# Optimization experiments

Measured on AMD Instinct MI355X. Metric: run time of the kernel, lower is better.

The kernel has to match this reference:

```python
import math
import jax, jax.numpy as jnp
import numpy as np

B, N, D, H = 16, 256, 1024, 16
DK = D // H
LAM_ATT, LAM_DIST = 0.33, 0.33
LAM_ADJ = 1.0 - LAM_ATT - LAM_DIST
EPS, NEG_INF = 1e-6, 1e12


def setup_inputs() -> dict:
    key = jax.random.key(0)
    ks = jax.random.split(key, 16)
    inp = {
        'query': jax.random.normal(ks[0], (B, N, D), jnp.float32),
        'key': jax.random.normal(ks[1], (B, N, D), jnp.float32),
        'value': jax.random.normal(ks[2], (B, N, D), jnp.float32),
        'adj_matrix': jax.random.uniform(ks[3], (B, N, N), jnp.float32),
        'distance_matrix': jax.random.uniform(ks[4], (B, N, N), jnp.float32),
        'edges_att': jnp.zeros((1,), jnp.float32),  # unused by forward
    }
    mask = jax.random.randint(ks[5], (B, N), 0, 2, jnp.int32)
    inp['mask'] = mask.at[:, 0].set(1)  # guarantee >=1 valid atom per graph
    scale = 0.02
    inp['Wq'] = jax.random.normal(ks[6], (D, D), jnp.float32) * scale
    inp['bq'] = jnp.zeros((D,), jnp.float32)
    inp['Wk'] = jax.random.normal(ks[7], (D, D), jnp.float32) * scale
    inp['bk'] = jnp.zeros((D,), jnp.float32)
    inp['Wv'] = jax.random.normal(ks[8], (D, D), jnp.float32) * scale
    inp['bv'] = jnp.zeros((D,), jnp.float32)
    inp['Wo'] = jax.random.normal(ks[9], (D, D), jnp.float32) * scale
    inp['bo'] = jnp.zeros((D,), jnp.float32)
    return inp


def reference(query, key, value, adj_matrix, distance_matrix, edges_att, mask,
              Wq, bq, Wk, bk, Wv, bv, Wo, bo):
    b, n, d = query.shape
    proj = lambda x, W, bias: (x @ W + bias).reshape(b, n, H, DK).transpose(0, 2, 1, 3)
    q = proj(query, Wq, bq)   # [B,H,N,DK]
    k = proj(key, Wk, bk)
    v = proj(value, Wv, bv)

    scores = jnp.einsum('bhqd,bhkd->bhqk', q, k) / math.sqrt(DK)
    key_invalid = (mask == 0)[:, None, None, :]          # [B,1,1,N]
    scores = jnp.where(key_invalid, -NEG_INF, scores)
    p_attn = jax.nn.softmax(scores, axis=-1)             # [B,H,N,N]

    # row-normalized adjacency (broadcast over heads instead of repeat)
    p_adj = adj_matrix / (adj_matrix.sum(axis=-1, keepdims=True) + EPS)  # [B,N,N]

    # distance kernel: softmax(-dist) with masked columns sent to +inf
    dist = jnp.where((mask == 0)[:, None, :], jnp.inf, distance_matrix)  # [B,N,N]
    p_dist = jax.nn.softmax(-dist, axis=-1)

    p_weighted = (LAM_ATT * p_attn
                  + LAM_DIST * p_dist[:, None]
                  + LAM_ADJ * p_adj[:, None])            # [B,H,N,N]
    # dropout p=0.0 -> identity

    x = jnp.einsum('bhqk,bhkd->bhqd', p_weighted, v)     # [B,H,N,DK]
    x = x.transpose(0, 2, 1, 3).reshape(b, n, d)
    return x @ Wo + bo
```

## Files before the change

### kernel.cpp

```cpp
#include <hip/hip_runtime.h>
#include <hip/hip_bf16.h>

typedef short short8 __attribute__((ext_vector_type(8)));
typedef short short4v __attribute__((ext_vector_type(4)));
typedef float floatx4 __attribute__((ext_vector_type(4)));

constexpr int BB  = 16;
constexpr int NN  = 256;
constexpr int DD  = 1024;
constexpr int HHc = 16;
constexpr int DKc = 64;

constexpr float LAM_ATT  = 0.33f;
constexpr float LAM_DIST = 0.33f;
constexpr float LAM_ADJ  = 0.34f;
constexpr float EPS_     = 1e-6f;

__device__ __forceinline__ float loadf(const void* p, size_t i, int f32) {
    return f32 ? ((const float*)p)[i] : (float)((const __hip_bfloat16*)p)[i];
}

__device__ __forceinline__ short8 load8_bf16(const void* p, size_t i, int f32) {
    if (f32) {
        const float4* q = (const float4*)((const float*)p + i);
        float4 a = q[0], b = q[1];
        short8 r;
        r[0] = (short)__bfloat16_as_ushort(__float2bfloat16(a.x));
        r[1] = (short)__bfloat16_as_ushort(__float2bfloat16(a.y));
        r[2] = (short)__bfloat16_as_ushort(__float2bfloat16(a.z));
        r[3] = (short)__bfloat16_as_ushort(__float2bfloat16(a.w));
        r[4] = (short)__bfloat16_as_ushort(__float2bfloat16(b.x));
        r[5] = (short)__bfloat16_as_ushort(__float2bfloat16(b.y));
        r[6] = (short)__bfloat16_as_ushort(__float2bfloat16(b.z));
        r[7] = (short)__bfloat16_as_ushort(__float2bfloat16(b.w));
        return r;
    }
    return *(const short8*)((const __hip_bfloat16*)p + i);
}

__device__ __forceinline__ void gl_lds16(const void* g, void* l) {
    __builtin_amdgcn_global_load_lds(
        (const __attribute__((address_space(1))) void*)g,
        (__attribute__((address_space(3))) void*)l, 16, 0, 0);
}

__global__ __launch_bounds__(256) void detect_kernel(
    const void* __restrict__ query, const void* __restrict__ maskraw,
    int* __restrict__ mask_canon, int* __restrict__ flags)
{
    __shared__ int s_f32;
    const int tid = threadIdx.x;
    if (tid == 0) s_f32 = 0;
    __syncthreads();

    const unsigned short* qh = (const unsigned short*)query;
    int hit = 0;
    for (int i = tid; i < 16384; i += 256)
        if ((qh[i] & 0x7F80u) == 0x7F80u) hit = 1;
    if (hit) atomicOr(&s_f32, 1);
    __syncthreads();
    if (tid == 0) flags[0] = s_f32;

    unsigned int w0 = ((const unsigned int*)maskraw)[0];
    int mdt = (w0 == 1u) ? 0 : ((w0 == 0x3F800000u) ? 1 : 2);

    for (int i = tid; i < BB * NN; i += 256) {
        int v;
        if (mdt == 0)      v = (((const int*)maskraw)[i] != 0);
        else if (mdt == 1) v = ((((const unsigned int*)maskraw)[i] & 0x7FFFFFFFu) != 0u);
        else               v = ((((const unsigned short*)maskraw)[i] & 0x7FFFu) != 0);
        mask_canon[i] = v;
    }
}

__global__ __launch_bounds__(256) void convert_acts(
    const void* q, const void* k, const void* v,
    __hip_bfloat16* __restrict__ Qc, __hip_bfloat16* __restrict__ Kc,
    __hip_bfloat16* __restrict__ Vc, const int* __restrict__ flags)
{
    const int f32 = flags[0];
    const int y = blockIdx.y;
    const void* src = (y == 0) ? q : (y == 1) ? k : v;
    __hip_bfloat16* dst = (y == 0) ? Qc : (y == 1) ? Kc : Vc;
    size_t off = ((size_t)blockIdx.x * 256 + threadIdx.x) * 8;
    *(short8*)(dst + off) = load8_bf16(src, off, f32);
}

__global__ __launch_bounds__(256) void prep_w(
    const void* W0, const void* W1, const void* W2, const void* W3,
    const int* __restrict__ flags, __hip_bfloat16* __restrict__ Wt_all)
{
    const int f32 = flags[0];
    const void* W = (blockIdx.z == 0) ? W0 : (blockIdx.z == 1) ? W1
                  : (blockIdx.z == 2) ? W2 : W3;
    __hip_bfloat16* Wt = Wt_all + (size_t)blockIdx.z * DD * DD;
    __shared__ __hip_bfloat16 T[64][66];
    const int k0 = blockIdx.y * 64, n0 = blockIdx.x * 64;
    #pragma unroll
    for (int i = 0; i < 16; i++) {
        int e = threadIdx.x + i * 256;
        int kr = e >> 6, nc = e & 63;
        T[kr][nc] = __float2bfloat16(loadf(W, (size_t)(k0 + kr) * DD + n0 + nc, f32));
    }
    __syncthreads();
    #pragma unroll
    for (int i = 0; i < 16; i++) {
        int e = threadIdx.x + i * 256;
        int nr = e >> 6, kc = e & 63;
        Wt[(size_t)(n0 + nr) * DD + k0 + kc] = T[kc][nr];
    }
}

__global__ __launch_bounds__(256) void prep_bias(
    const void* b0, const void* b1, const void* b2, const void* b3,
    const int* __restrict__ flags, __hip_bfloat16* __restrict__ bias_all)
{
    const int f32 = flags[0];
    const void* s = (blockIdx.x == 0) ? b0 : (blockIdx.x == 1) ? b1
                  : (blockIdx.x == 2) ? b2 : b3;
    #pragma unroll
    for (int i = 0; i < 4; i++) {
        int idx = threadIdx.x + i * 256;
        bias_all[blockIdx.x * DD + idx] = __float2bfloat16(loadf(s, idx, f32));
    }
}

__global__ __launch_bounds__(256) void mix_kernel(
    const void* __restrict__ adj, const void* __restrict__ dist,
    const int* __restrict__ mask_canon, const int* __restrict__ flags,
    __hip_bfloat16* __restrict__ Mmix)
{
    const int f32 = flags[0];
    const int wave = threadIdx.x >> 6, lane = threadIdx.x & 63;
    const int b = blockIdx.y;
    const int q = blockIdx.x * 4 + wave;
    const size_t rowOff = ((size_t)b * NN + q) * NN;
    const int c0 = lane * 4;

    float a[4], nd[4];
    int msk[4];
    #pragma unroll
    for (int i = 0; i < 4; i++) {
        a[i]   = loadf(adj, rowOff + c0 + i, f32);
        msk[i] = mask_canon[b * NN + c0 + i];
        nd[i]  = msk[i] ? -loadf(dist, rowOff + c0 + i, f32) : -3.0e38f;
    }

    float asum = a[0] + a[1] + a[2] + a[3];
    #pragma unroll
    for (int off = 1; off < 64; off <<= 1) asum += __shfl_xor(asum, off);

    float mx = fmaxf(fmaxf(nd[0], nd[1]), fmaxf(nd[2], nd[3]));
    #pragma unroll
    for (int off = 1; off < 64; off <<= 1) mx = fmaxf(mx, __shfl_xor(mx, off));

    float e[4];
    float esum = 0.f;
    #pragma unroll
    for (int i = 0; i < 4; i++) {
        e[i] = msk[i] ? __expf(nd[i] - mx) : 0.f;
        esum += e[i];
    }
    #pragma unroll
    for (int off = 1; off < 64; off <<= 1) esum += __shfl_xor(esum, off);

    const float ia = 1.f / (asum + EPS_);
    const float ie = 1.f / fmaxf(esum, 1e-30f);
    __hip_bfloat16 out[4];
    #pragma unroll
    for (int i = 0; i < 4; i++)
        out[i] = __float2bfloat16(LAM_DIST * e[i] * ie + LAM_ADJ * a[i] * ia);
    *(short4v*)((unsigned short*)Mmix + rowOff + c0) = *(short4v*)out;
}

template<int MSUB, int NSUB>
__device__ __forceinline__ void gemm_core(
    const __hip_bfloat16* __restrict__ A,
    const __hip_bfloat16* __restrict__ Wt,
    const __hip_bfloat16* __restrict__ bias,
    void* __restrict__ C,
    int c_f32, int rowBase, int colBase,
    __hip_bfloat16* __restrict__ Vt, int writeVt)
{
    constexpr int BM = 32 * MSUB, BN = 32 * NSUB;
    __shared__ __hip_bfloat16 As[BM][32];
    __shared__ __hip_bfloat16 Ws[BN][32];

    const int tid  = threadIdx.x;
    const int wave = tid >> 6, lane = tid & 63;
    const int quad = lane >> 4, cl = lane & 15;
    const int wm = (wave >> 1) * (16 * MSUB), wn = (wave & 1) * (16 * NSUB);
    const int lr = lane >> 2;
    const int lc = (lane & 3) * 8;

    floatx4 acc[MSUB][NSUB];
    #pragma unroll
    for (int i = 0; i < MSUB; i++)
        #pragma unroll
        for (int j = 0; j < NSUB; j++)
            acc[i][j] = (floatx4){0.f, 0.f, 0.f, 0.f};

    for (int k0 = 0; k0 < DD; k0 += 32) {
        #pragma unroll
        for (int j = 0; j < MSUB / 2; j++) {
            int r0 = (wave * (MSUB / 2) + j) * 16;
            gl_lds16(A + (size_t)(rowBase + r0 + lr) * DD + k0 + lc, &As[r0][0]);
        }
        #pragma unroll
        for (int j = 0; j < NSUB / 2; j++) {
            int r0 = (wave * (NSUB / 2) + j) * 16;
            gl_lds16(Wt + (size_t)(colBase + r0 + lr) * DD + k0 + lc, &Ws[r0][0]);
        }
        __syncthreads();

        short8 af[MSUB], bfr[NSUB];
        #pragma unroll
        for (int ms = 0; ms < MSUB; ms++)
            af[ms] = *(const short8*)&As[wm + ms * 16 + cl][quad * 8];
        #pragma unroll
        for (int ns = 0; ns < NSUB; ns++)
            bfr[ns] = *(const short8*)&Ws[wn + ns * 16 + cl][quad * 8];
        #pragma unroll
        for (int ms = 0; ms < MSUB; ms++)
            #pragma unroll
            for (int ns = 0; ns < NSUB; ns++)
                acc[ms][ns] = __builtin_amdgcn_mfma_f32_16x16x32_bf16(
                    af[ms], bfr[ns], acc[ms][ns], 0, 0, 0);
        __syncthreads();
    }

    #pragma unroll
    for (int ns = 0; ns < NSUB; ns++) {
        int col = colBase + wn + ns * 16 + cl;
        float bc = (float)bias[col];
        if (writeVt) {
            int h = col >> 6, dk = col & 63;
            #pragma unroll
            for (int ms = 0; ms < MSUB; ms++) {
                int row0 = rowBase + wm + ms * 16 + quad * 4;
                int b = row0 >> 8, tok = row0 & 255;
                __hip_bfloat16 pk[4];
                #pragma unroll
                for (int r = 0; r < 4; r++)
                    pk[r] = __float2bfloat16(acc[ms][ns][r] + bc);
                *(short4v*)&Vt[((size_t)((b * HHc + h) * DKc + dk)) * NN + tok] =
                    *(short4v*)pk;
            }
        } else {
            #pragma unroll
            for (int ms = 0; ms < MSUB; ms++) {
                #pragma unroll
                for (int r = 0; r < 4; r++) {
                    int row = rowBase + wm + ms * 16 + quad * 4 + r;
                    float v = acc[ms][ns][r] + bc;
                    size_t idx = (size_t)row * DD + col;
                    if (c_f32) ((float*)C)[idx] = v;
                    else ((__hip_bfloat16*)C)[idx] = __float2bfloat16(v);
                }
            }
        }
    }
}

__global__ __launch_bounds__(256) void qkv_mfma(
    const __hip_bfloat16* __restrict__ Qc, const __hip_bfloat16* __restrict__ Kc,
    const __hip_bfloat16* __restrict__ Vc,
    const __hip_bfloat16* __restrict__ Wt_all,
    const __hip_bfloat16* __restrict__ bias_all,
    __hip_bfloat16* Qp, __hip_bfloat16* Kp, __hip_bfloat16* Vt)
{
    const int bid = blockIdx.x;
    const int xcd = bid & 7, s = bid >> 3;
    const int x = s & 7;
    const int t = s >> 3;
    const int y = xcd + 8 * (t & 3);
    const int z = t >> 2;

    const __hip_bfloat16* A = (z == 0) ? Qc : (z == 1) ? Kc : Vc;
    __hip_bfloat16* C = (z == 0) ? Qp : Kp;
    gemm_core<4, 4>(A, Wt_all + (size_t)z * DD * DD, bias_all + z * DD, C,
                    0, y * 128, x * 128, Vt, z == 2);
}

__global__ __launch_bounds__(256) void out_mfma(
    const __hip_bfloat16* __restrict__ X,
    const __hip_bfloat16* __restrict__ Wt,
    const __hip_bfloat16* __restrict__ bias,
    void* C, const int* __restrict__ flags)
{
    const int bid = blockIdx.x;
    const int xcd = bid & 7, s = bid >> 3;
    const int x = s & 15;
    const int y = xcd + 8 * (s >> 4);
    gemm_core<4, 2>(X, Wt, bias, C, flags[0], y * 128, x * 64, nullptr, 0);
}

__global__ __launch_bounds__(256) void attn_mfma(
    const __hip_bfloat16* __restrict__ Qp,
    const __hip_bfloat16* __restrict__ Kp,
    const __hip_bfloat16* __restrict__ Vt,
    const __hip_bfloat16* __restrict__ Mmix,
    const int* __restrict__ mask_canon,
    __hip_bfloat16* __restrict__ X)
{
    __shared__ __hip_bfloat16 smem[16896];
    __hip_bfloat16* Ks = smem;
    __hip_bfloat16* Ps = smem;

    const int bid = blockIdx.x;
    const int xcd = bid & 7, sdec = bid >> 3;
    const int qt = sdec & 3;
    const int hb = xcd + 8 * (sdec >> 2);
    const int h = hb & 15, b = hb >> 4;

    const int tid = threadIdx.x;
    const int wave = tid >> 6, lane = tid & 63;
    const int quad = lane >> 4, cl = lane & 15;
    const int q0 = qt * 64 + wave * 16;

    const size_t qoff = ((size_t)(b * NN + q0 + cl)) * DD + h * DKc + quad * 8;
    short8 aq0 = *(const short8*)(Qp + qoff);
    short8 aq1 = *(const short8*)(Qp + qoff + 32);

    #pragma unroll
    for (int j = 0; j < 8; j++) {
        int cbase = (j * 4 + wave) * 64;
        int c = cbase + lane;
        int tok = c >> 3, kc = c & 7;
        gl_lds16(Kp + ((size_t)(b * NN + tok)) * DD + h * DKc + ((kc ^ (tok & 7)) * 8),
                 (char*)Ks + (size_t)cbase * 16);
    }

    int msk[16];
    #pragma unroll
    for (int ns = 0; ns < 16; ns++)
        msk[ns] = mask_canon[b * NN + ns * 16 + cl];

    __syncthreads();

    floatx4 accS[16];
    #pragma unroll
    for (int ns = 0; ns < 16; ns++) accS[ns] = (floatx4){0.f, 0.f, 0.f, 0.f};
    #pragma unroll
    for (int ns = 0; ns < 16; ns++) {
        int tok = ns * 16 + cl;
        const __hip_bfloat16* row = Ks + tok * 64;
        short8 bk0 = *(const short8*)(row + ((quad ^ (tok & 7)) * 8));
        short8 bk1 = *(const short8*)(row + (((quad + 4) ^ (tok & 7)) * 8));
        accS[ns] = __builtin_amdgcn_mfma_f32_16x16x32_bf16(aq0, bk0, accS[ns], 0, 0, 0);
        accS[ns] = __builtin_amdgcn_mfma_f32_16x16x32_bf16(aq1, bk1, accS[ns], 0, 0, 0);
    }
    __syncthreads();

    #pragma unroll
    for (int r = 0; r < 4; r++) {
        float s[16];
        #pragma unroll
        for (int ns = 0; ns < 16; ns++)
            s[ns] = msk[ns] ? accS[ns][r] * 0.125f : -1e12f;
        float mx = s[0];
        #pragma unroll
        for (int ns = 1; ns < 16; ns++) mx = fmaxf(mx, s[ns]);
        mx = fmaxf(mx, __shfl_xor(mx, 1));
        mx = fmaxf(mx, __shfl_xor(mx, 2));
        mx = fmaxf(mx, __shfl_xor(mx, 4));
        mx = fmaxf(mx, __shfl_xor(mx, 8));
        float e[16], sum = 0.f;
        #pragma unroll
        for (int ns = 0; ns < 16; ns++) {
            e[ns] = msk[ns] ? __expf(s[ns] - mx) : 0.f;
            sum += e[ns];
        }
        sum += __shfl_xor(sum, 1);
        sum += __shfl_xor(sum, 2);
        sum += __shfl_xor(sum, 4);
        sum += __shfl_xor(sum, 8);
        float inv = LAM_ATT / sum;
        const size_t mrow = ((size_t)b * NN + q0 + quad * 4 + r) * NN;
        #pragma unroll
        for (int ns = 0; ns < 16; ns++) {
            float p = e[ns] * inv + (float)Mmix[mrow + ns * 16 + cl];
            Ps[(wave * 16 + quad * 4 + r) * 264 + ns * 16 + cl] = __float2bfloat16(p);
        }
    }
    __syncthreads();

    floatx4 accX[4];
    #pragma unroll
    for (int nd = 0; nd < 4; nd++) accX[nd] = (floatx4){0.f, 0.f, 0.f, 0.f};
    #pragma unroll
    for (int ks = 0; ks < 8; ks++) {
        short8 ap = *(const short8*)&Ps[(wave * 16 + cl) * 264 + ks * 32 + quad * 8];
        #pragma unroll
        for (int nd = 0; nd < 4; nd++) {
            const size_t voff = ((size_t)((b * HHc + h) * DKc + nd * 16 + cl)) * NN
                              + ks * 32 + quad * 8;
            short8 bv = *(const short8*)(Vt + voff);
            accX[nd] = __builtin_amdgcn_mfma_f32_16x16x32_bf16(ap, bv, accX[nd], 0, 0, 0);
        }
    }
    #pragma unroll
    for (int nd = 0; nd < 4; nd++) {
        #pragma unroll
        for (int r = 0; r < 4; r++) {
            int row = b * NN + q0 + quad * 4 + r;
            X[(size_t)row * DD + h * DKc + nd * 16 + cl] = __float2bfloat16(accX[nd][r]);
        }
    }
}

extern "C" void kernel_launch(void* const* d_in, const int* in_sizes, int n_in,
                              void* d_out, int out_size, void* d_ws, size_t ws_size,
                              hipStream_t stream)
{
    const void* query   = d_in[0];
    const void* key     = d_in[1];
    const void* value   = d_in[2];
    const void* adj     = d_in[3];
    const void* dist    = d_in[4];
    const void* maskraw = d_in[6];
    const void* Wq = d_in[7];   const void* bq = d_in[8];
    const void* Wk = d_in[9];   const void* bk = d_in[10];
    const void* Wv = d_in[11];  const void* bv = d_in[12];
    const void* Wo = d_in[13];  const void* bo = d_in[14];

    char* w = (char*)d_ws;
    int* mask_canon = (int*)w;
    int* flags      = (int*)(w + 16384);
    __hip_bfloat16* Wt_all   = (__hip_bfloat16*)(w + 32768);
    __hip_bfloat16* bias_all = (__hip_bfloat16*)(w + 32768 + ((size_t)8 << 20));
    char* base2 = w + 32768 + ((size_t)8 << 20) + 32768;
    const size_t tokElems = (size_t)BB * NN * DD;
    __hip_bfloat16* Qc   = (__hip_bfloat16*)base2;
    __hip_bfloat16* Kc   = Qc + tokElems;
    __hip_bfloat16* Vc   = Kc + tokElems;
    __hip_bfloat16* Qp   = Vc + tokElems;
    __hip_bfloat16* Kp   = Qp + tokElems;
    __hip_bfloat16* Vt   = Kp + tokElems;
    __hip_bfloat16* Mmix = Vt + tokElems;
    __hip_bfloat16* X    = Qc;

    detect_kernel<<<1, 256, 0, stream>>>(query, maskraw, mask_canon, flags);
    convert_acts<<<dim3(2048, 3), 256, 0, stream>>>(query, key, value, Qc, Kc, Vc, flags);
    prep_w<<<dim3(16, 16, 4), 256, 0, stream>>>(Wq, Wk, Wv, Wo, flags, Wt_all);
    prep_bias<<<dim3(4), 256, 0, stream>>>(bq, bk, bv, bo, flags, bias_all);
    mix_kernel<<<dim3(NN / 4, BB), 256, 0, stream>>>(adj, dist, mask_canon, flags, Mmix);

    qkv_mfma<<<768, 256, 0, stream>>>(Qc, Kc, Vc, Wt_all, bias_all, Qp, Kp, Vt);

    attn_mfma<<<1024, 256, 0, stream>>>(Qp, Kp, Vt, Mmix, mask_canon, X);

    out_mfma<<<512, 256, 0, stream>>>(X, Wt_all + (size_t)3 * DD * DD,
                                      bias_all + 3 * DD, d_out, flags);
}
```

Before: 257.6 us.

## Merge prep kernels into one launch and deepen GEMM K-tile with swizzled LDS

After: 249.4 us. 3.2% less time.

```diff
diff --git a/kernel.cpp b/kernel.cpp
--- a/kernel.cpp
+++ b/kernel.cpp
@@ -73,104 +73,99 @@
     }
 }
 
-__global__ __launch_bounds__(256) void convert_acts(
-    const void* q, const void* k, const void* v,
+__global__ __launch_bounds__(256) void prep_mega(
+    const void* query, const void* key, const void* value,
+    const void* adj, const void* dist,
+    const void* W0, const void* W1, const void* W2, const void* W3,
+    const void* b0, const void* b1, const void* b2, const void* b3,
+    const int* __restrict__ mask_canon, const int* __restrict__ flags,
+    __hip_bfloat16* __restrict__ Wt_all, __hip_bfloat16* __restrict__ bias_all,
+    __hip_bfloat16* __restrict__ Mmix,
     __hip_bfloat16* __restrict__ Qc, __hip_bfloat16* __restrict__ Kc,
-    __hip_bfloat16* __restrict__ Vc, const int* __restrict__ flags)
-{
+    __hip_bfloat16* __restrict__ Vc)
+{
+    __shared__ __hip_bfloat16 T[64][66];
     const int f32 = flags[0];
-    const int y = blockIdx.y;
-    const void* src = (y == 0) ? q : (y == 1) ? k : v;
-    __hip_bfloat16* dst = (y == 0) ? Qc : (y == 1) ? Kc : Vc;
-    size_t off = ((size_t)blockIdx.x * 256 + threadIdx.x) * 8;
-    *(short8*)(dst + off) = load8_bf16(src, off, f32);
-}
-
-__global__ __launch_bounds__(256) void prep_w(
-    const void* W0, const void* W1, const void* W2, const void* W3,
-    const int* __restrict__ flags, __hip_bfloat16* __restrict__ Wt_all)
-{
-    const int f32 = flags[0];
-    const void* W = (blockIdx.z == 0) ? W0 : (blockIdx.z == 1) ? W1
-                  : (blockIdx.z == 2) ? W2 : W3;
-    __hip_bfloat16* Wt = Wt_all + (size_t)blockIdx.z * DD * DD;
-    __shared__ __hip_bfloat16 T[64][66];
-    const int k0 = blockIdx.y * 64, n0 = blockIdx.x * 64;
-    #pragma unroll
-    for (int i = 0; i < 16; i++) {
-        int e = threadIdx.x + i * 256;
-        int kr = e >> 6, nc = e & 63;
-        T[kr][nc] = __float2bfloat16(loadf(W, (size_t)(k0 + kr) * DD + n0 + nc, f32));
-    }
-    __syncthreads();
-    #pragma unroll
-    for (int i = 0; i < 16; i++) {
-        int e = threadIdx.x + i * 256;
-        int nr = e >> 6, kc = e & 63;
-        Wt[(size_t)(n0 + nr) * DD + k0 + kc] = T[kc][nr];
-    }
-}
-
-__global__ __launch_bounds__(256) void prep_bias(
-    const void* b0, const void* b1, const void* b2, const void* b3,
-    const int* __restrict__ flags, __hip_bfloat16* __restrict__ bias_all)
-{
-    const int f32 = flags[0];
-    const void* s = (blockIdx.x == 0) ? b0 : (blockIdx.x == 1) ? b1
-                  : (blockIdx.x == 2) ? b2 : b3;
-    #pragma unroll
-    for (int i = 0; i < 4; i++) {
-        int idx = threadIdx.x + i * 256;
-        bias_all[blockIdx.x * DD + idx] = __float2bfloat16(loadf(s, idx, f32));
-    }
-}
-
-__global__ __launch_bounds__(256) void mix_kernel(
-    const void* __restrict__ adj, const void* __restrict__ dist,
-    const int* __restrict__ mask_canon, const int* __restrict__ flags,
-    __hip_bfloat16* __restrict__ Mmix)
-{
-    const int f32 = flags[0];
-    const int wave = threadIdx.x >> 6, lane = threadIdx.x & 63;
-    const int b = blockIdx.y;
-    const int q = blockIdx.x * 4 + wave;
-    const size_t rowOff = ((size_t)b * NN + q) * NN;
-    const int c0 = lane * 4;
-
-    float a[4], nd[4];
-    int msk[4];
-    #pragma unroll
-    for (int i = 0; i < 4; i++) {
-        a[i]   = loadf(adj, rowOff + c0 + i, f32);
-        msk[i] = mask_canon[b * NN + c0 + i];
-        nd[i]  = msk[i] ? -loadf(dist, rowOff + c0 + i, f32) : -3.0e38f;
-    }
-
-    float asum = a[0] + a[1] + a[2] + a[3];
-    #pragma unroll
-    for (int off = 1; off < 64; off <<= 1) asum += __shfl_xor(asum, off);
-
-    float mx = fmaxf(fmaxf(nd[0], nd[1]), fmaxf(nd[2], nd[3]));
-    #pragma unroll
-    for (int off = 1; off < 64; off <<= 1) mx = fmaxf(mx, __shfl_xor(mx, off));
-
-    float e[4];
-    float esum = 0.f;
-    #pragma unroll
-    for (int i = 0; i < 4; i++) {
-        e[i] = msk[i] ? __expf(nd[i] - mx) : 0.f;
-        esum += e[i];
-    }
-    #pragma unroll
-    for (int off = 1; off < 64; off <<= 1) esum += __shfl_xor(esum, off);
-
-    const float ia = 1.f / (asum + EPS_);
-    const float ie = 1.f / fmaxf(esum, 1e-30f);
-    __hip_bfloat16 out[4];
-    #pragma unroll
-    for (int i = 0; i < 4; i++)
-        out[i] = __float2bfloat16(LAM_DIST * e[i] * ie + LAM_ADJ * a[i] * ia);
-    *(short4v*)((unsigned short*)Mmix + rowOff + c0) = *(short4v*)out;
+    const int bid = blockIdx.x;
+    const int tid = threadIdx.x;
+
+    if (bid < 1024) {
+        const int z = bid >> 8, rem = bid & 255;
+        const int y = rem >> 4, x = rem & 15;
+        const void* W = (z == 0) ? W0 : (z == 1) ? W1 : (z == 2) ? W2 : W3;
+        __hip_bfloat16* Wt = Wt_all + (size_t)z * DD * DD;
+        const int k0 = y * 64, n0 = x * 64;
+        #pragma unroll
+        for (int i = 0; i < 16; i++) {
+            int e = tid + i * 256;
+            int kr = e >> 6, nc = e & 63;
+            T[kr][nc] = __float2bfloat16(loadf(W, (size_t)(k0 + kr) * DD + n0 + nc, f32));
+        }
+        __syncthreads();
+        #pragma unroll
+        for (int i = 0; i < 16; i++) {
+            int e = tid + i * 256;
+            int nr = e >> 6, kc = e & 63;
+            Wt[(size_t)(n0 + nr) * DD + k0 + kc] = T[kc][nr];
+        }
+    } else if (bid < 1028) {
+        const int z = bid - 1024;
+        const void* s = (z == 0) ? b0 : (z == 1) ? b1 : (z == 2) ? b2 : b3;
+        #pragma unroll
+        for (int i = 0; i < 4; i++) {
+            int idx = tid + i * 256;
+            bias_all[z * DD + idx] = __float2bfloat16(loadf(s, idx, f32));
+        }
+    } else if (bid < 2052) {
+        const int idx = bid - 1028;
+        const int wave = tid >> 6, lane = tid & 63;
+        const int b = idx >> 6;
+        const int q = (idx & 63) * 4 + wave;
+        const size_t rowOff = ((size_t)b * NN + q) * NN;
+        const int c0 = lane * 4;
+
+        float a[4], nd[4];
+        int msk[4];
+        #pragma unroll
+        for (int i = 0; i < 4; i++) {
+            a[i]   = loadf(adj, rowOff + c0 + i, f32);
+            msk[i] = mask_canon[b * NN + c0 + i];
+            nd[i]  = msk[i] ? -loadf(dist, rowOff + c0 + i, f32) : -3.0e38f;
+        }
+
+        float asum = a[0] + a[1] + a[2] + a[3];
+        #pragma unroll
+        for (int off = 1; off < 64; off <<= 1) asum += __shfl_xor(asum, off);
+
+        float mx = fmaxf(fmaxf(nd[0], nd[1]), fmaxf(nd[2], nd[3]));
+        #pragma unroll
+        for (int off = 1; off < 64; off <<= 1) mx = fmaxf(mx, __shfl_xor(mx, off));
+
+        float e[4];
+        float esum = 0.f;
+        #pragma unroll
+        for (int i = 0; i < 4; i++) {
+            e[i] = msk[i] ? __expf(nd[i] - mx) : 0.f;
+            esum += e[i];
+        }
+        #pragma unroll
+        for (int off = 1; off < 64; off <<= 1) esum += __shfl_xor(esum, off);
+
+        const float ia = 1.f / (asum + EPS_);
+        const float ie = 1.f / fmaxf(esum, 1e-30f);
+        __hip_bfloat16 out[4];
+        #pragma unroll
+        for (int i = 0; i < 4; i++)
+            out[i] = __float2bfloat16(LAM_DIST * e[i] * ie + LAM_ADJ * a[i] * ia);
+        *(short4v*)((unsigned short*)Mmix + rowOff + c0) = *(short4v*)out;
+    } else {
+        const int idx = bid - 2052;
+        const int y = idx >> 11, xb = idx & 2047;
+        const void* src = (y == 0) ? query : (y == 1) ? key : value;
+        __hip_bfloat16* dst = (y == 0) ? Qc : (y == 1) ? Kc : Vc;
+        size_t off = ((size_t)xb * 256 + tid) * 8;
+        *(short8*)(dst + off) = load8_bf16(src, off, f32);
+    }
 }
 
 template<int MSUB, int NSUB>
@@ -183,15 +178,15 @@
     __hip_bfloat16* __restrict__ Vt, int writeVt)
 {
     constexpr int BM = 32 * MSUB, BN = 32 * NSUB;
-    __shared__ __hip_bfloat16 As[BM][32];
-    __shared__ __hip_bfloat16 Ws[BN][32];
+    __shared__ __hip_bfloat16 As[BM][64];
+    __shared__ __hip_bfloat16 Ws[BN][64];
 
     const int tid  = threadIdx.x;
     const int wave = tid >> 6, lane = tid & 63;
     const int quad = lane >> 4, cl = lane & 15;
     const int wm = (wave >> 1) * (16 * MSUB), wn = (wave & 1) * (16 * NSUB);
-    const int lr = lane >> 2;
-    const int lc = (lane & 3) * 8;
+    const int srow = lane >> 3;
+    const int spos = lane & 7;
 
     floatx4 acc[MSUB][NSUB];
     #pragma unroll
@@ -200,32 +195,45 @@
         for (int j = 0; j < NSUB; j++)
             acc[i][j] = (floatx4){0.f, 0.f, 0.f, 0.f};
 
-    for (int k0 = 0; k0 < DD; k0 += 32) {
-        #pragma unroll
-        for (int j = 0; j < MSUB / 2; j++) {
-            int r0 = (wave * (MSUB / 2) + j) * 16;
-            gl_lds16(A + (size_t)(rowBase + r0 + lr) * DD + k0 + lc, &As[r0][0]);
-        }
-        #pragma unroll
-        for (int j = 0; j < NSUB / 2; j++) {
-            int r0 = (wave * (NSUB / 2) + j) * 16;
-            gl_lds16(Wt + (size_t)(colBase + r0 + lr) * DD + k0 + lc, &Ws[r0][0]);
+    for (int k0 = 0; k0 < DD; k0 += 64) {
+        #pragma unroll
+        for (int j = 0; j < BM / 32; j++) {
+            int r0 = wave * (BM / 4) + j * 8;
+            int row = r0 + srow;
+            int g = spos ^ (row & 7);
+            gl_lds16(A + (size_t)(rowBase + row) * DD + k0 + g * 8, &As[r0][0]);
+        }
+        #pragma unroll
+        for (int j = 0; j < BN / 32; j++) {
+            int r0 = wave * (BN / 4) + j * 8;
+            int row = r0 + srow;
+            int g = spos ^ (row & 7);
+            gl_lds16(Wt + (size_t)(colBase + row) * DD + k0 + g * 8, &Ws[r0][0]);
         }
         __syncthreads();
 
-        short8 af[MSUB], bfr[NSUB];
-        #pragma unroll
-        for (int ms = 0; ms < MSUB; ms++)
-            af[ms] = *(const short8*)&As[wm + ms * 16 + cl][quad * 8];
-        #pragma unroll
-        for (int ns = 0; ns < NSUB; ns++)
-            bfr[ns] = *(const short8*)&Ws[wn + ns * 16 + cl][quad * 8];
-        #pragma unroll
-        for (int ms = 0; ms < MSUB; ms++)
+        #pragma unroll
+        for (int kh = 0; kh < 2; kh++) {
+            short8 af[MSUB], bfr[NSUB];
             #pragma unroll
-            for (int ns = 0; ns < NSUB; ns++)
-                acc[ms][ns] = __builtin_amdgcn_mfma_f32_16x16x32_bf16(
-                    af[ms], bfr[ns], acc[ms][ns], 0, 0, 0);
+            for (int ms = 0; ms < MSUB; ms++) {
+                int row = wm + ms * 16 + cl;
+                int p = (kh * 4 + quad) ^ (row & 7);
+                af[ms] = *(const short8*)&As[row][p * 8];
+            }
+            #pragma unroll
+            for (int ns = 0; ns < NSUB; ns++) {
+                int row = wn + ns * 16 + cl;
+                int p = (kh * 4 + quad) ^ (row & 7);
+                bfr[ns] = *(const short8*)&Ws[row][p * 8];
+            }
+            #pragma unroll
+            for (int ms = 0; ms < MSUB; ms++)
+                #pragma unroll
+                for (int ns = 0; ns < NSUB; ns++)
+                    acc[ms][ns] = __builtin_amdgcn_mfma_f32_16x16x32_bf16(
+                        af[ms], bfr[ns], acc[ms][ns], 0, 0, 0);
+        }
         __syncthreads();
     }
 
@@ -441,10 +449,11 @@
     __hip_bfloat16* X    = Qc;
 
     detect_kernel<<<1, 256, 0, stream>>>(query, maskraw, mask_canon, flags);
-    convert_acts<<<dim3(2048, 3), 256, 0, stream>>>(query, key, value, Qc, Kc, Vc, flags);
-    prep_w<<<dim3(16, 16, 4), 256, 0, stream>>>(Wq, Wk, Wv, Wo, flags, Wt_all);
-    prep_bias<<<dim3(4), 256, 0, stream>>>(bq, bk, bv, bo, flags, bias_all);
-    mix_kernel<<<dim3(NN / 4, BB), 256, 0, stream>>>(adj, dist, mask_canon, flags, Mmix);
+
+    prep_mega<<<8196, 256, 0, stream>>>(query, key, value, adj, dist,
+                                        Wq, Wk, Wv, Wo, bq, bk, bv, bo,
+                                        mask_canon, flags,
+                                        Wt_all, bias_all, Mmix, Qc, Kc, Vc);
 
     qkv_mfma<<<768, 256, 0, stream>>>(Qc, Kc, Vc, Wt_all, bias_all, Qp, Kp, Vt);
 
```
